# Optimization experiments

Measured on AMD Instinct MI355X. Metric: run time of the kernel, lower is better.

## Reference

```python
import jax, jax.numpy as jnp
import numpy as np

IN_DIM, OUT_DIM, HID, L, PRED_LEN = 6, 6, 512, 4, 10


def _rnn_layer(x, Wih, Whh, bih, bhh):
    """Vanilla tanh RNN layer, batch_first x: [B,T,D] -> ([B,T,H], hT [B,H])."""
    B = x.shape[0]
    H = Whh.shape[0]
    xW = jnp.einsum('btd,hd->bth', x, Wih) + bih  # precompute input projections

    def step(h, xw_t):
        h = jnp.tanh(xw_t + h @ Whh.T + bhh)
        return h, h

    h0 = jnp.zeros((B, H), x.dtype)
    hT, ys = jax.lax.scan(step, h0, jnp.swapaxes(xW, 0, 1))
    return jnp.swapaxes(ys, 0, 1), hT


def setup_inputs() -> dict:
    key = jax.random.key(0)
    ks = jax.random.split(key, 16)
    s_in = 1.0 / np.sqrt(HID)
    u = lambda k, shp: jax.random.uniform(k, shp, jnp.float32, -s_in, s_in)
    inp = {
        'x': jax.random.normal(ks[0], (1024, 128, IN_DIM), jnp.float32),
        # encoder RNN params (layer 0 has input_dim=6, layers 1..3 have HID)
        'enc_Wih0': u(ks[1], (HID, IN_DIM)),
        'enc_Wih': u(ks[2], (L - 1, HID, HID)),
        'enc_Whh': u(ks[3], (L, HID, HID)),
        'enc_bih': u(ks[4], (L, HID)),
        'enc_bhh': u(ks[5], (L, HID)),
        # decoder RNN params (all layers take HID-dim input)
        'dec_Wih': u(ks[6], (L, HID, HID)),
        'dec_Whh': u(ks[7], (L, HID, HID)),
        'dec_bih': u(ks[8], (L, HID)),
        'dec_bhh': u(ks[9], (L, HID)),
        # output head
        'fc_W': u(ks[10], (OUT_DIM, HID)),
        'fc_b': u(ks[11], (OUT_DIM,)),
    }
    return inp


def reference(x, enc_Wih0, enc_Wih, enc_Whh, enc_bih, enc_bhh,
              dec_Wih, dec_Whh, dec_bih, dec_bhh, fc_W, fc_b):
    B = x.shape[0]
    # ---- encoder: 4-layer tanh RNN over src sequence ----
    h_enc = []
    out = x
    for l in range(L):
        Wih = enc_Wih0 if l == 0 else enc_Wih[l - 1]
        out, hT = _rnn_layer(out, Wih, enc_Whh[l], enc_bih[l], enc_bhh[l])
        h_enc.append(hT)
    enc_outputs = out                      # [B, T_src, HID]
    hidden = jnp.stack(h_enc)              # [L, B, HID]

    de_input0 = enc_outputs[:, -1, :]      # [B, HID]

    def dec_step(carry, _):
        inp, h = carry
        x_l = inp
        new_h = []
        for l in range(L):
            hl = jnp.tanh(x_l @ dec_Wih[l].T + dec_bih[l]
                          + h[l] @ dec_Whh[l].T + dec_bhh[l])
            new_h.append(hl)
            x_l = hl
        return (x_l, jnp.stack(new_h)), x_l

    _, ys = jax.lax.scan(dec_step, (de_input0, hidden), None, length=PRED_LEN)
    dec_out = jnp.swapaxes(ys, 0, 1)       # [B, PRED_LEN, HID]
    outputs = dec_out @ fc_W.T + fc_b      # [B, PRED_LEN, OUT_DIM]
    return enc_outputs, outputs
```

## Files before the change

### kernel.cpp

```cpp
#include <hip/hip_runtime.h>

typedef _Float16 f16;
typedef _Float16 f16x8 __attribute__((ext_vector_type(8)));
typedef float    f32x4 __attribute__((ext_vector_type(4)));

#define TSEQ 128
#define PRED 10

__global__ void k_cvt(const float* __restrict__ src, f16* __restrict__ dst, int n) {
  int i = blockIdx.x * blockDim.x + threadIdx.x;
  int stride = gridDim.x * blockDim.x;
  for (; i < n; i += stride) dst[i] = (f16)src[i];
}

__global__ void k_bias(const float* __restrict__ a, const float* __restrict__ b,
                       float* __restrict__ o, int n) {
  int i = blockIdx.x * blockDim.x + threadIdx.x;
  if (i < n) o[i] = a[i] + b[i];
}

__global__ __launch_bounds__(256) void k_gemm_xw(
    const f16* __restrict__ A, const f16* __restrict__ W,
    const float* __restrict__ bias, f16* __restrict__ C) {
  __shared__ f16 As[128 * 72];
  __shared__ f16 Bs[256 * 72];
  const int tid = threadIdx.x;
  const int w = tid >> 6, lane = tid & 63;
  const int wm = w >> 1, wn = w & 1;
  const int q = lane >> 4, l15 = lane & 15;
  const int m0 = blockIdx.x * 128;
  const int n0 = blockIdx.y * 256;

  f32x4 acc[4][8];
  const f32x4 zero = {0.f, 0.f, 0.f, 0.f};
#pragma unroll
  for (int i = 0; i < 4; i++)
#pragma unroll
    for (int j = 0; j < 8; j++) acc[i][j] = zero;

  for (int k0 = 0; k0 < 512; k0 += 64) {
    __syncthreads();
#pragma unroll
    for (int i = 0; i < 4; i++) {
      int ch = tid + 256 * i; int r = ch >> 3, kc = ch & 7;
      *(f16x8*)&As[r * 72 + kc * 8] = *(const f16x8*)&A[(size_t)(m0 + r) * 512 + k0 + kc * 8];
    }
#pragma unroll
    for (int i = 0; i < 8; i++) {
      int ch = tid + 256 * i; int r = ch >> 3, kc = ch & 7;
      *(f16x8*)&Bs[r * 72 + kc * 8] = *(const f16x8*)&W[(size_t)(n0 + r) * 512 + k0 + kc * 8];
    }
    __syncthreads();
#pragma unroll
    for (int kk = 0; kk < 2; kk++) {
      f16x8 af[4], bf[8];
#pragma unroll
      for (int mt = 0; mt < 4; mt++)
        af[mt] = *(const f16x8*)&As[(wm * 64 + mt * 16 + l15) * 72 + kk * 32 + q * 8];
#pragma unroll
      for (int nt = 0; nt < 8; nt++)
        bf[nt] = *(const f16x8*)&Bs[(wn * 128 + nt * 16 + l15) * 72 + kk * 32 + q * 8];
#pragma unroll
      for (int mt = 0; mt < 4; mt++)
#pragma unroll
        for (int nt = 0; nt < 8; nt++)
          acc[mt][nt] = __builtin_amdgcn_mfma_f32_16x16x32_f16(af[mt], bf[nt], acc[mt][nt], 0, 0, 0);
    }
  }
#pragma unroll
  for (int mt = 0; mt < 4; mt++)
#pragma unroll
    for (int nt = 0; nt < 8; nt++)
#pragma unroll
      for (int r = 0; r < 4; r++) {
        int mg = m0 + wm * 64 + mt * 16 + q * 4 + r;
        int ng = n0 + wn * 128 + nt * 16 + l15;
        C[(size_t)mg * 512 + ng] = (f16)(acc[mt][nt][r] + bias[ng]);
      }
}

__global__ __launch_bounds__(256) void k_enc_rec(
    const f16* __restrict__ xw, const float* __restrict__ x,
    const float* __restrict__ Wih0, const float* __restrict__ bias0,
    const f16* __restrict__ Whh, f16* __restrict__ out_h,
    float* __restrict__ out_f, f16* __restrict__ hT,
    f16* __restrict__ hx, int* __restrict__ ctr, int is_l0) {
  __shared__ f16 As[16 * 520];
  __shared__ float xs[16][8];
  const int tid = threadIdx.x;
  const int w = tid >> 6, lane = tid & 63, q = lane >> 4, l15 = lane & 15;
  const int c = blockIdx.x & 63, sub = blockIdx.x >> 6;
  const int row0 = c * 16;
  const int ncol0 = sub * 128 + w * 32;
  int* myctr = ctr + c * 32;

  f16x8 Bfr[2][16];
#pragma unroll
  for (int t2 = 0; t2 < 2; t2++) {
    int ng = ncol0 + t2 * 16 + l15;
#pragma unroll
    for (int kk = 0; kk < 16; kk++)
      Bfr[t2][kk] = *(const f16x8*)&Whh[(size_t)ng * 512 + kk * 32 + q * 8];
  }

  float w0[2][6]; float b0[2];
  if (is_l0) {
#pragma unroll
    for (int t2 = 0; t2 < 2; t2++) {
      int ng = ncol0 + t2 * 16 + l15;
#pragma unroll
      for (int d = 0; d < 6; d++) w0[t2][d] = Wih0[ng * 6 + d];
      b0[t2] = bias0[ng];
    }
  }

  for (int i = tid; i < 16 * 520; i += 256) As[i] = (f16)0.0f;
  if (is_l0 && tid < 96) xs[tid / 6][tid % 6] = x[(size_t)(row0 + tid / 6) * TSEQ * 6 + tid % 6];
  __syncthreads();

  for (int t = 0; t < TSEQ; t++) {
    const int p = t & 1;
    f16 xwr[2][4];
    if (!is_l0) {
#pragma unroll
      for (int t2 = 0; t2 < 2; t2++)
#pragma unroll
        for (int r = 0; r < 4; r++)
          xwr[t2][r] = xw[((size_t)(row0 + q * 4 + r) * TSEQ + t) * 512 + ncol0 + t2 * 16 + l15];
    }

    const f32x4 zero = {0.f, 0.f, 0.f, 0.f};
    f32x4 acc0 = zero, acc1 = zero;
#pragma unroll
    for (int kk = 0; kk < 16; kk++) {
      f16x8 a = *(const f16x8*)&As[l15 * 520 + kk * 32 + q * 8];
      acc0 = __builtin_amdgcn_mfma_f32_16x16x32_f16(a, Bfr[0][kk], acc0, 0, 0, 0);
      acc1 = __builtin_amdgcn_mfma_f32_16x16x32_f16(a, Bfr[1][kk], acc1, 0, 0, 0);
    }

#pragma unroll
    for (int t2 = 0; t2 < 2; t2++) {
      f32x4 accv = t2 ? acc1 : acc0;
      int ng = ncol0 + t2 * 16 + l15;
      union { unsigned long long u; f16 h4[4]; } pk;
      float hv[4];
#pragma unroll
      for (int r = 0; r < 4; r++) {
        int m = q * 4 + r;
        float pre;
        if (is_l0) {
          float xwv = b0[t2];
#pragma unroll
          for (int d = 0; d < 6; d++) xwv += xs[m][d] * w0[t2][d];
          pre = accv[r] + xwv;
        } else {
          pre = accv[r] + (float)xwr[t2][r];
        }
        hv[r] = tanhf(pre);
        pk.h4[r] = (f16)hv[r];
      }
      if (t < TSEQ - 1)
        __hip_atomic_store(
            (unsigned long long*)&hx[(((size_t)p * 64 + c) * 512 + ng) * 16 + q * 4],
            pk.u, __ATOMIC_RELAXED, __HIP_MEMORY_SCOPE_AGENT);
#pragma unroll
      for (int r = 0; r < 4; r++) {
        int b = row0 + q * 4 + r;
        out_h[((size_t)b * TSEQ + t) * 512 + ng] = pk.h4[r];
        if (out_f) out_f[((size_t)b * TSEQ + t) * 512 + ng] = hv[r];
        if (t == TSEQ - 1) hT[(size_t)b * 512 + ng] = pk.h4[r];
      }
    }
    if (t == TSEQ - 1) break;

    __builtin_amdgcn_s_waitcnt(0);
    __syncthreads();
    if (tid == 0) {
      __hip_atomic_fetch_add(myctr, 1, __ATOMIC_RELAXED, __HIP_MEMORY_SCOPE_AGENT);
      int target = 4 * (t + 1);
      while (__hip_atomic_load(myctr, __ATOMIC_RELAXED, __HIP_MEMORY_SCOPE_AGENT) < target)
        __builtin_amdgcn_s_sleep(1);
    }
    __syncthreads();

    {
      unsigned long long v[8];
#pragma unroll
      for (int cc = 0; cc < 2; cc++) {
        int col = tid * 2 + cc;
        const unsigned long long* bp =
            (const unsigned long long*)&hx[(((size_t)p * 64 + c) * 512 + col) * 16];
#pragma unroll
        for (int j = 0; j < 4; j++)
          v[cc * 4 + j] = __hip_atomic_load(bp + j, __ATOMIC_RELAXED, __HIP_MEMORY_SCOPE_AGENT);
      }
#pragma unroll
      for (int cc = 0; cc < 2; cc++) {
        int col = tid * 2 + cc;
        union { unsigned long long u[4]; f16 h[16]; } un;
        un.u[0] = v[cc * 4]; un.u[1] = v[cc * 4 + 1];
        un.u[2] = v[cc * 4 + 2]; un.u[3] = v[cc * 4 + 3];
#pragma unroll
        for (int k = 0; k < 16; k++) As[k * 520 + col] = un.h[k];
      }
    }
    if (is_l0 && tid < 96)
      xs[tid / 6][tid % 6] = x[((size_t)(row0 + tid / 6) * TSEQ + (t + 1)) * 6 + tid % 6];
    __syncthreads();
  }
}

__global__ __launch_bounds__(256) void k_dec_rec(
    const f16* __restrict__ Wih, const f16* __restrict__ Whh,
    const float* __restrict__ decB, const f16* __restrict__ hT,
    f16* __restrict__ hstate, f16* __restrict__ dec_out, int* __restrict__ ctr) {
  __shared__ f16 xb[16 * 520];
  __shared__ f16 hb[16 * 520];
  const int tid = threadIdx.x;
  const int w = tid >> 6, lane = tid & 63, q = lane >> 4, l15 = lane & 15;
  const int c = blockIdx.x & 63, sub = blockIdx.x >> 6;
  const int row0 = c * 16;
  const int ncol0 = sub * 128 + w * 32;
  int* myctr = ctr + c * 32;
  const size_t LSZ = (size_t)1024 * 512;

  auto load_rm = [&](f16* dst, const f16* src) {
#pragma unroll
    for (int i = 0; i < 4; i++) {
      int idx = tid + 256 * i; int m = idx >> 6, kc = idx & 63;
      *(f16x8*)&dst[m * 520 + kc * 8] = *(const f16x8*)&src[(size_t)(row0 + m) * 512 + kc * 8];
    }
  };
  auto load_cm = [&](f16* dst, int buf) {
    unsigned long long v[8];
#pragma unroll
    for (int cc = 0; cc < 2; cc++) {
      int col = tid * 2 + cc;
      const unsigned long long* bp =
          (const unsigned long long*)&hstate[(((size_t)buf * 64 + c) * 512 + col) * 16];
#pragma unroll
      for (int j = 0; j < 4; j++)
        v[cc * 4 + j] = __hip_atomic_load(bp + j, __ATOMIC_RELAXED, __HIP_MEMORY_SCOPE_AGENT);
    }
#pragma unroll
    for (int cc = 0; cc < 2; cc++) {
      int col = tid * 2 + cc;
      union { unsigned long long u[4]; f16 h[16]; } un;
      un.u[0] = v[cc * 4]; un.u[1] = v[cc * 4 + 1];
      un.u[2] = v[cc * 4 + 2]; un.u[3] = v[cc * 4 + 3];
#pragma unroll
      for (int k = 0; k < 16; k++) dst[k * 520 + col] = un.h[k];
    }
  };

  for (int s = 0; s < PRED; s++) {
    int wb = (s + 1) & 1, rb = s & 1;
    for (int l = 0; l < 4; l++) {
      if (l == 0) {
        if (s == 0) load_rm(xb, hT + 3 * LSZ);
        else load_cm(xb, rb * 4 + 3);
      } else {
        load_cm(xb, wb * 4 + (l - 1));
      }
      if (s == 0) load_rm(hb, hT + (size_t)l * LSZ);
      else load_cm(hb, rb * 4 + l);
      __syncthreads();

      const f32x4 zero = {0.f, 0.f, 0.f, 0.f};
      f32x4 acc0 = zero, acc1 = zero;
      const f16* Wl = Wih + (size_t)l * 512 * 512;
      const f16* Ul = Whh + (size_t)l * 512 * 512;
      int ng0 = ncol0 + l15, ng1 = ncol0 + 16 + l15;
#pragma unroll
      for (int kk = 0; kk < 16; kk++) {
        f16x8 a = *(const f16x8*)&xb[l15 * 520 + kk * 32 + q * 8];
        f16x8 bv0 = *(const f16x8*)&Wl[(size_t)ng0 * 512 + kk * 32 + q * 8];
        f16x8 bv1 = *(const f16x8*)&Wl[(size_t)ng1 * 512 + kk * 32 + q * 8];
        acc0 = __builtin_amdgcn_mfma_f32_16x16x32_f16(a, bv0, acc0, 0, 0, 0);
        acc1 = __builtin_amdgcn_mfma_f32_16x16x32_f16(a, bv1, acc1, 0, 0, 0);
      }
#pragma unroll
      for (int kk = 0; kk < 16; kk++) {
        f16x8 a = *(const f16x8*)&hb[l15 * 520 + kk * 32 + q * 8];
        f16x8 bv0 = *(const f16x8*)&Ul[(size_t)ng0 * 512 + kk * 32 + q * 8];
        f16x8 bv1 = *(const f16x8*)&Ul[(size_t)ng1 * 512 + kk * 32 + q * 8];
        acc0 = __builtin_amdgcn_mfma_f32_16x16x32_f16(a, bv0, acc0, 0, 0, 0);
        acc1 = __builtin_amdgcn_mfma_f32_16x16x32_f16(a, bv1, acc1, 0, 0, 0);
      }

      int obuf = wb * 4 + l;
#pragma unroll
      for (int t2 = 0; t2 < 2; t2++) {
        f32x4 accv = t2 ? acc1 : acc0;
        int ng = ncol0 + t2 * 16 + l15;
        union { unsigned long long u; f16 h4[4]; } pk;
#pragma unroll
        for (int r = 0; r < 4; r++)
          pk.h4[r] = (f16)tanhf(accv[r] + decB[l * 512 + ng]);
        __hip_atomic_store(
            (unsigned long long*)&hstate[(((size_t)obuf * 64 + c) * 512 + ng) * 16 + q * 4],
            pk.u, __ATOMIC_RELAXED, __HIP_MEMORY_SCOPE_AGENT);
        if (l == 3) {
#pragma unroll
          for (int r = 0; r < 4; r++)
            dec_out[((size_t)(row0 + q * 4 + r) * PRED + s) * 512 + ng] = pk.h4[r];
        }
      }
      __builtin_amdgcn_s_waitcnt(0);
      __syncthreads();
      if (tid == 0) {
        __hip_atomic_fetch_add(myctr, 1, __ATOMIC_RELAXED, __HIP_MEMORY_SCOPE_AGENT);
        int target = 4 * (s * 4 + l + 1);
        while (__hip_atomic_load(myctr, __ATOMIC_RELAXED, __HIP_MEMORY_SCOPE_AGENT) < target)
          __builtin_amdgcn_s_sleep(1);
      }
      __syncthreads();
    }
  }
}

__global__ __launch_bounds__(256) void k_fc(
    const f16* __restrict__ dec_out, const float* __restrict__ fcW,
    const float* __restrict__ fcb, float* __restrict__ out) {
  __shared__ float Wl[6 * 512];
  __shared__ float bl[8];
  int tid = threadIdx.x;
  for (int i = tid; i < 3072; i += 256) Wl[i] = fcW[i];
  if (tid < 6) bl[tid] = fcb[tid];
  __syncthreads();
  int g = blockIdx.x * 256 + tid;
  const f16* row = dec_out + (size_t)g * 512;
  float acc[6] = {0, 0, 0, 0, 0, 0};
  for (int kc = 0; kc < 64; kc++) {
    f16x8 xv = *(const f16x8*)&row[kc * 8];
#pragma unroll
    for (int j = 0; j < 8; j++) {
      float xf = (float)xv[j];
#pragma unroll
      for (int o = 0; o < 6; o++) acc[o] += xf * Wl[o * 512 + kc * 8 + j];
    }
  }
#pragma unroll
  for (int o = 0; o < 6; o++) out[(size_t)g * 6 + o] = acc[o] + bl[o];
}

extern "C" void kernel_launch(void* const* d_in, const int* in_sizes, int n_in,
                              void* d_out, int out_size, void* d_ws, size_t ws_size,
                              hipStream_t stream) {
  const float* x      = (const float*)d_in[0];
  const float* Wih0   = (const float*)d_in[1];
  const float* eWih32 = (const float*)d_in[2];
  const float* eWhh32 = (const float*)d_in[3];
  const float* ebih   = (const float*)d_in[4];
  const float* ebhh   = (const float*)d_in[5];
  const float* dWih32 = (const float*)d_in[6];
  const float* dWhh32 = (const float*)d_in[7];
  const float* dbih   = (const float*)d_in[8];
  const float* dbhh   = (const float*)d_in[9];
  const float* fcW    = (const float*)d_in[10];
  const float* fcb    = (const float*)d_in[11];
  float* outp = (float*)d_out;

  char* ws = (char*)d_ws;
  size_t off = 0;
  auto alloc = [&](size_t bytes) { void* p = ws + off; off += (bytes + 255) & ~255ULL; return p; };
  f16* outA   = (f16*)alloc((size_t)131072 * 512 * 2);
  f16* xwB    = (f16*)alloc((size_t)131072 * 512 * 2);
  f16* eWih   = (f16*)alloc((size_t)3 * 262144 * 2);
  f16* eWhh   = (f16*)alloc((size_t)4 * 262144 * 2);
  f16* dWih   = (f16*)alloc((size_t)4 * 262144 * 2);
  f16* dWhh   = (f16*)alloc((size_t)4 * 262144 * 2);
  float* encB = (float*)alloc(2048 * 4);
  float* decB = (float*)alloc(2048 * 4);
  f16* hT     = (f16*)alloc((size_t)4 * 1024 * 512 * 2);
  f16* hstate = (f16*)alloc((size_t)8 * 1024 * 512 * 2);
  f16* hx     = (f16*)alloc((size_t)2 * 1024 * 512 * 2);
  f16* dec_o  = (f16*)alloc((size_t)1024 * 10 * 512 * 2);
  int* ctr    = (int*)alloc(5 * 64 * 32 * 4);

  hipMemsetAsync(ctr, 0, 5 * 64 * 32 * 4, stream);
  k_cvt<<<512, 256, 0, stream>>>(eWih32, eWih, 3 * 262144);
  k_cvt<<<512, 256, 0, stream>>>(eWhh32, eWhh, 4 * 262144);
  k_cvt<<<512, 256, 0, stream>>>(dWih32, dWih, 4 * 262144);
  k_cvt<<<512, 256, 0, stream>>>(dWhh32, dWhh, 4 * 262144);
  k_bias<<<8, 256, 0, stream>>>(ebih, ebhh, encB, 2048);
  k_bias<<<8, 256, 0, stream>>>(dbih, dbhh, decB, 2048);

  k_enc_rec<<<256, 256, 0, stream>>>(nullptr, x, Wih0, encB, eWhh, outA, nullptr, hT, hx, ctr, 1);
  for (int l = 1; l < 4; l++) {
    k_gemm_xw<<<dim3(1024, 2), 256, 0, stream>>>(outA, eWih + (size_t)(l - 1) * 262144,
                                                 encB + l * 512, xwB);
    float* of = (l == 3) ? outp : nullptr;
    k_enc_rec<<<256, 256, 0, stream>>>(xwB, nullptr, nullptr, nullptr,
                                       eWhh + (size_t)l * 262144, outA, of,
                                       hT + (size_t)l * 524288, hx, ctr + l * 2048, 0);
  }
  k_dec_rec<<<256, 256, 0, stream>>>(dWih, dWhh, decB, hT, hstate, dec_o, ctr + 4 * 2048);
  k_fc<<<40, 256, 0, stream>>>(dec_o, fcW, fcb, outp + (size_t)1024 * 128 * 512);
}
```

Before: 3.434 ms.

## Signal step completion before bulk output writes; pack LDS transposes; regroup decoder blocks

In both the encoder recurrence and the decoder, each block now stores its hidden-state slice, bumps the shared counter, and only then writes the large out_h/out_f/dec_out outputs. The global-memory stores therefore overlap with waiting for peer blocks instead of sitting on the critical path before the barrier. The column-major-to-LDS transpose now writes packed 32-bit pairs instead of single f16 values, halving the LDS store count. The decoder block index mapping is changed so the four column sub-blocks of a batch group get adjacent block IDs, and the final decoder step skips its needless sync.

```diff
diff --git a/kernel.cpp b/kernel.cpp
--- a/kernel.cpp
+++ b/kernel.cpp
@@ -3,6 +3,7 @@
 typedef _Float16 f16;
 typedef _Float16 f16x8 __attribute__((ext_vector_type(8)));
 typedef float    f32x4 __attribute__((ext_vector_type(4)));
+typedef unsigned long long u64;
 
 #define TSEQ 128
 #define PRED 10
@@ -138,12 +139,11 @@
       acc1 = __builtin_amdgcn_mfma_f32_16x16x32_f16(a, Bfr[1][kk], acc1, 0, 0, 0);
     }
 
+    float hv[2][4];
+    union { u64 u; f16 h4[4]; } pk[2];
 #pragma unroll
     for (int t2 = 0; t2 < 2; t2++) {
       f32x4 accv = t2 ? acc1 : acc0;
-      int ng = ncol0 + t2 * 16 + l15;
-      union { unsigned long long u; f16 h4[4]; } pk;
-      float hv[4];
 #pragma unroll
       for (int r = 0; r < 4; r++) {
         int m = q * 4 + r;
@@ -156,27 +156,39 @@
         } else {
           pre = accv[r] + (float)xwr[t2][r];
         }
-        hv[r] = tanhf(pre);
-        pk.h4[r] = (f16)hv[r];
-      }
-      if (t < TSEQ - 1)
+        hv[t2][r] = tanhf(pre);
+        pk[t2].h4[r] = (f16)hv[t2][r];
+      }
+    }
+
+    if (t < TSEQ - 1) {
+#pragma unroll
+      for (int t2 = 0; t2 < 2; t2++) {
+        int ng = ncol0 + t2 * 16 + l15;
         __hip_atomic_store(
-            (unsigned long long*)&hx[(((size_t)p * 64 + c) * 512 + ng) * 16 + q * 4],
-            pk.u, __ATOMIC_RELAXED, __HIP_MEMORY_SCOPE_AGENT);
+            (u64*)&hx[(((size_t)p * 64 + c) * 512 + ng) * 16 + q * 4],
+            pk[t2].u, __ATOMIC_RELAXED, __HIP_MEMORY_SCOPE_AGENT);
+      }
+      __builtin_amdgcn_s_waitcnt(0);
+      __syncthreads();
+      if (tid == 0)
+        __hip_atomic_fetch_add(myctr, 1, __ATOMIC_RELAXED, __HIP_MEMORY_SCOPE_AGENT);
+    }
+
+#pragma unroll
+    for (int t2 = 0; t2 < 2; t2++) {
+      int ng = ncol0 + t2 * 16 + l15;
 #pragma unroll
       for (int r = 0; r < 4; r++) {
         int b = row0 + q * 4 + r;
-        out_h[((size_t)b * TSEQ + t) * 512 + ng] = pk.h4[r];
-        if (out_f) out_f[((size_t)b * TSEQ + t) * 512 + ng] = hv[r];
-        if (t == TSEQ - 1) hT[(size_t)b * 512 + ng] = pk.h4[r];
+        out_h[((size_t)b * TSEQ + t) * 512 + ng] = pk[t2].h4[r];
+        if (out_f) out_f[((size_t)b * TSEQ + t) * 512 + ng] = hv[t2][r];
+        if (t == TSEQ - 1) hT[(size_t)b * 512 + ng] = pk[t2].h4[r];
       }
     }
     if (t == TSEQ - 1) break;
 
-    __builtin_amdgcn_s_waitcnt(0);
-    __syncthreads();
     if (tid == 0) {
-      __hip_atomic_fetch_add(myctr, 1, __ATOMIC_RELAXED, __HIP_MEMORY_SCOPE_AGENT);
       int target = 4 * (t + 1);
       while (__hip_atomic_load(myctr, __ATOMIC_RELAXED, __HIP_MEMORY_SCOPE_AGENT) < target)
         __builtin_amdgcn_s_sleep(1);
@@ -184,24 +196,23 @@
     __syncthreads();
 
     {
-      unsigned long long v[8];
+      u64 v[8];
 #pragma unroll
       for (int cc = 0; cc < 2; cc++) {
         int col = tid * 2 + cc;
-        const unsigned long long* bp =
-            (const unsigned long long*)&hx[(((size_t)p * 64 + c) * 512 + col) * 16];
+        const u64* bp = (const u64*)&hx[(((size_t)p * 64 + c) * 512 + col) * 16];
 #pragma unroll
         for (int j = 0; j < 4; j++)
           v[cc * 4 + j] = __hip_atomic_load(bp + j, __ATOMIC_RELAXED, __HIP_MEMORY_SCOPE_AGENT);
       }
-#pragma unroll
-      for (int cc = 0; cc < 2; cc++) {
-        int col = tid * 2 + cc;
-        union { unsigned long long u[4]; f16 h[16]; } un;
-        un.u[0] = v[cc * 4]; un.u[1] = v[cc * 4 + 1];
-        un.u[2] = v[cc * 4 + 2]; un.u[3] = v[cc * 4 + 3];
-#pragma unroll
-        for (int k = 0; k < 16; k++) As[k * 520 + col] = un.h[k];
+      union { u64 u[4]; f16 h[16]; } un0, un1;
+      un0.u[0] = v[0]; un0.u[1] = v[1]; un0.u[2] = v[2]; un0.u[3] = v[3];
+      un1.u[0] = v[4]; un1.u[1] = v[5]; un1.u[2] = v[6]; un1.u[3] = v[7];
+#pragma unroll
+      for (int k = 0; k < 16; k++) {
+        union { f16 h2[2]; unsigned int u; } pw;
+        pw.h2[0] = un0.h[k]; pw.h2[1] = un1.h[k];
+        *(unsigned int*)&As[k * 520 + tid * 2] = pw.u;
       }
     }
     if (is_l0 && tid < 96)
@@ -218,7 +229,7 @@
   __shared__ f16 hb[16 * 520];
   const int tid = threadIdx.x;
   const int w = tid >> 6, lane = tid & 63, q = lane >> 4, l15 = lane & 15;
-  const int c = blockIdx.x & 63, sub = blockIdx.x >> 6;
+  const int c = blockIdx.x >> 2, sub = blockIdx.x & 3;
   const int row0 = c * 16;
   const int ncol0 = sub * 128 + w * 32;
   int* myctr = ctr + c * 32;
@@ -232,30 +243,30 @@
     }
   };
   auto load_cm = [&](f16* dst, int buf) {
-    unsigned long long v[8];
+    u64 v[8];
 #pragma unroll
     for (int cc = 0; cc < 2; cc++) {
       int col = tid * 2 + cc;
-      const unsigned long long* bp =
-          (const unsigned long long*)&hstate[(((size_t)buf * 64 + c) * 512 + col) * 16];
+      const u64* bp = (const u64*)&hstate[(((size_t)buf * 64 + c) * 512 + col) * 16];
 #pragma unroll
       for (int j = 0; j < 4; j++)
         v[cc * 4 + j] = __hip_atomic_load(bp + j, __ATOMIC_RELAXED, __HIP_MEMORY_SCOPE_AGENT);
     }
-#pragma unroll
-    for (int cc = 0; cc < 2; cc++) {
-      int col = tid * 2 + cc;
-      union { unsigned long long u[4]; f16 h[16]; } un;
-      un.u[0] = v[cc * 4]; un.u[1] = v[cc * 4 + 1];
-      un.u[2] = v[cc * 4 + 2]; un.u[3] = v[cc * 4 + 3];
-#pragma unroll
-      for (int k = 0; k < 16; k++) dst[k * 520 + col] = un.h[k];
+    union { u64 u[4]; f16 h[16]; } un0, un1;
+    un0.u[0] = v[0]; un0.u[1] = v[1]; un0.u[2] = v[2]; un0.u[3] = v[3];
+    un1.u[0] = v[4]; un1.u[1] = v[5]; un1.u[2] = v[6]; un1.u[3] = v[7];
+#pragma unroll
+    for (int k = 0; k < 16; k++) {
+      union { f16 h2[2]; unsigned int u; } pw;
+      pw.h2[0] = un0.h[k]; pw.h2[1] = un1.h[k];
+      *(unsigned int*)&dst[k * 520 + tid * 2] = pw.u;
     }
   };
 
   for (int s = 0; s < PRED; s++) {
     int wb = (s + 1) & 1, rb = s & 1;
     for (int l = 0; l < 4; l++) {
+      const bool last = (s == PRED - 1) && (l == 3);
       if (l == 0) {
         if (s == 0) load_rm(xb, hT + 3 * LSZ);
         else load_cm(xb, rb * 4 + 3);
@@ -289,32 +300,48 @@
       }
 
       int obuf = wb * 4 + l;
+      union { u64 u; f16 h4[4]; } pk[2];
 #pragma unroll
       for (int t2 = 0; t2 < 2; t2++) {
         f32x4 accv = t2 ? acc1 : acc0;
         int ng = ncol0 + t2 * 16 + l15;
-        union { unsigned long long u; f16 h4[4]; } pk;
 #pragma unroll
         for (int r = 0; r < 4; r++)
-          pk.h4[r] = (f16)tanhf(accv[r] + decB[l * 512 + ng]);
-        __hip_atomic_store(
-            (unsigned long long*)&hstate[(((size_t)obuf * 64 + c) * 512 + ng) * 16 + q * 4],
-            pk.u, __ATOMIC_RELAXED, __HIP_MEMORY_SCOPE_AGENT);
-        if (l == 3) {
+          pk[t2].h4[r] = (f16)tanhf(accv[r] + decB[l * 512 + ng]);
+      }
+
+      if (!last) {
+#pragma unroll
+        for (int t2 = 0; t2 < 2; t2++) {
+          int ng = ncol0 + t2 * 16 + l15;
+          __hip_atomic_store(
+              (u64*)&hstate[(((size_t)obuf * 64 + c) * 512 + ng) * 16 + q * 4],
+              pk[t2].u, __ATOMIC_RELAXED, __HIP_MEMORY_SCOPE_AGENT);
+        }
+        __builtin_amdgcn_s_waitcnt(0);
+        __syncthreads();
+        if (tid == 0)
+          __hip_atomic_fetch_add(myctr, 1, __ATOMIC_RELAXED, __HIP_MEMORY_SCOPE_AGENT);
+      }
+
+      if (l == 3) {
+#pragma unroll
+        for (int t2 = 0; t2 < 2; t2++) {
+          int ng = ncol0 + t2 * 16 + l15;
 #pragma unroll
           for (int r = 0; r < 4; r++)
-            dec_out[((size_t)(row0 + q * 4 + r) * PRED + s) * 512 + ng] = pk.h4[r];
+            dec_out[((size_t)(row0 + q * 4 + r) * PRED + s) * 512 + ng] = pk[t2].h4[r];
         }
       }
-      __builtin_amdgcn_s_waitcnt(0);
-      __syncthreads();
-      if (tid == 0) {
-        __hip_atomic_fetch_add(myctr, 1, __ATOMIC_RELAXED, __HIP_MEMORY_SCOPE_AGENT);
-        int target = 4 * (s * 4 + l + 1);
-        while (__hip_atomic_load(myctr, __ATOMIC_RELAXED, __HIP_MEMORY_SCOPE_AGENT) < target)
-          __builtin_amdgcn_s_sleep(1);
-      }
-      __syncthreads();
+
+      if (!last) {
+        if (tid == 0) {
+          int target = 4 * (s * 4 + l + 1);
+          while (__hip_atomic_load(myctr, __ATOMIC_RELAXED, __HIP_MEMORY_SCOPE_AGENT) < target)
+            __builtin_amdgcn_s_sleep(1);
+        }
+        __syncthreads();
+      }
     }
   }
 }
```

Result: faster. 3.156 ms (-8.1%).
